# Kernel tuning notes

Hardware: AMD Instinct MI355X
Metric: run time of the kernel (lower is better)

## Reference

```python
import jax, jax.numpy as jnp
import numpy as np

B, T, C, H, K = 2, 4096, 2048, 32, 64
DM, DD, DA = 32, 64, 96
CHUNK = 128
NC = T // CHUNK
GN_EPS = 1e-5 * 8.0 ** 2  # eps * head_size_divisor**2


def setup_inputs() -> dict:
    key = jax.random.key(0)
    ks = iter(jax.random.split(key, 40))
    def nrm(shape, s=1.0):
        return jax.random.normal(next(ks), shape, dtype=jnp.float32) * s
    def uni(shape, lo, hi):
        return jax.random.uniform(next(ks), shape, dtype=jnp.float32, minval=lo, maxval=hi)
    return {
        "x": nrm((B, T, C)),
        "shift_state_in": nrm((B, C)),
        "wkv_state_in": jnp.zeros((B, H, K, K), dtype=jnp.float32),
        "time_maa_x": uni((1, 1, C), 0.0, 1.0),
        "time_maa_w": uni((1, 1, C), 0.0, 1.0),
        "time_maa_k": uni((1, 1, C), 0.0, 1.0),
        "time_maa_v": uni((1, 1, C), 0.0, 1.0),
        "time_maa_r": uni((1, 1, C), 0.0, 1.0),
        "time_maa_g": uni((1, 1, C), 0.0, 1.0),
        "time_maa_a": uni((1, 1, C), 0.0, 1.0),
        "time_maa_w1": nrm((C, 6 * DM), 0.01),
        "time_maa_w2": uni((6, DM, C), -0.01, 0.01),
        "time_decay": uni((1, 1, C), -6.0, -1.0),
        "time_decay_w1": nrm((C, DD), 0.02),
        "time_decay_w2": uni((DD, C), -0.01, 0.01),
        "time_faaaa": nrm((H, K), 0.1),
        "a0": nrm((1, 1, C), 0.01),
        "a1": nrm((C, DA), 0.02),
        "a2": nrm((DA, C), 0.1 / np.sqrt(DA)),
        "k_k": jnp.full((1, 1, C), 0.85, dtype=jnp.float32),
        "k_a": jnp.ones((1, 1, C), dtype=jnp.float32),
        "W_r": nrm((C, C), 1.0 / np.sqrt(C)),
        "W_k": nrm((C, C), 1.0 / np.sqrt(C)),
        "W_v": nrm((C, C), 1.0 / np.sqrt(C)),
        "W_g": nrm((C, C), 1.0 / np.sqrt(C)),
        "W_o": nrm((C, C), 1.0 / np.sqrt(C)),
        "gn_weight": jnp.ones((C,), dtype=jnp.float32),
        "gn_bias": jnp.zeros((C,), dtype=jnp.float32),
    }


def _wkv_delta(r, k, v, w_neg, u, kk, iclr, state0):
    # r,k,v,w_neg,kk,iclr: [B,T,C]; u: [H,K]; state0: [B,H,K,K]
    def to_chunks(t):  # [B,T,C] -> [NC,B,H,CHUNK,K]
        return t.reshape(B, NC, CHUNK, H, K).transpose(1, 0, 3, 2, 4)
    chunks = tuple(map(to_chunks, (r, k, v, w_neg, kk, iclr)))
    u4 = u.reshape(1, H, 1, K)
    mid = CHUNK // 2
    tri = jnp.tril(jnp.ones((CHUNK, CHUNK), dtype=bool), -1)
    eye = jnp.eye(CHUNK, dtype=jnp.float32)

    def step(state, chunk):
        r_c, k_c, v_c, w_log, kk_c, iclr_c = chunk
        w_cum = jnp.cumsum(w_log, axis=2)                       # [B,H,cs,K]
        w_cs = jnp.pad(w_cum[:, :, :-1, :], ((0, 0), (0, 0), (1, 0), (0, 0)))
        offset = w_cs[:, :, mid:mid + 1, :]
        r_decay = jnp.exp(jnp.clip(w_cs - offset, -30, 30))
        k_inv = jnp.exp(jnp.clip(offset - w_cum, -30, 30))
        A = jnp.einsum('bhtk,bhsk->bhts', r_c * r_decay, k_c * k_inv)
        A = jnp.where(tri, A, 0.0)
        diag = jnp.einsum('bhtk,bhtk->bht', r_c, u4 * k_c)
        A = A + diag[..., None] * eye                           # diag_embed add
        kk_corr = jnp.einsum('bhtk,bhsk->bhts', kk_c * iclr_c, kk_c)
        kk_corr = jnp.where(tri, kk_corr, 0.0)
        A_total = A - jnp.tril(A @ kk_corr)
        w_intra = jnp.exp(jnp.clip(w_cum - w_log, -30, 30))
        y = A_total @ v_c + (r_c * w_intra) @ state             # [B,H,cs,K]
        wsum = jnp.sum(w_log, axis=2, keepdims=True)            # [B,H,1,K]
        ws = jnp.exp(wsum)
        w_inter = jnp.exp(jnp.clip(wsum - w_cum, -30, 30))
        kv = jnp.einsum('bhtk,bhtv->bhkv', k_c * w_inter, v_c)
        ab = jnp.einsum('bhtk,bhtj->bhkj', -kk_c * w_inter, kk_c * iclr_c)
        state = state * ws + state @ ab + kv                    # ws broadcasts on dim -2, as in torch
        return state, y

    state, ys = jax.lax.scan(step, state0.astype(jnp.float32), chunks)
    out = ys.transpose(1, 0, 3, 2, 4).reshape(B, T, C)
    return out, state


def reference(x, shift_state_in, wkv_state_in, time_maa_x, time_maa_w, time_maa_k,
              time_maa_v, time_maa_r, time_maa_g, time_maa_a, time_maa_w1, time_maa_w2,
              time_decay, time_decay_w1, time_decay_w2, time_faaaa, a0, a1, a2,
              k_k, k_a, W_r, W_k, W_v, W_g, W_o, gn_weight, gn_bias):
    dxprev = jnp.concatenate([shift_state_in[:, None, :], x[:, :-1]], axis=1) - x
    xxx = jnp.tanh((x + dxprev * time_maa_x) @ time_maa_w1)     # [B,T,6*DM]
    m = jnp.einsum('btsd,sdc->sbtc', xxx.reshape(B, T, 6, DM), time_maa_w2)
    mw, mk, mv, mr, mg, ma = m
    xw = x + dxprev * (time_maa_w + mw)
    xk = x + dxprev * (time_maa_k + mk)
    xv = x + dxprev * (time_maa_v + mv)
    xr = x + dxprev * (time_maa_r + mr)
    xg = x + dxprev * (time_maa_g + mg)
    xa = x + dxprev * (time_maa_a + ma)
    r = xr @ W_r
    k = xk @ W_k
    v = xv @ W_v
    g = jax.nn.silu(xg @ W_g)
    w = time_decay + jnp.tanh(xw @ time_decay_w1) @ time_decay_w2
    iclr = jax.nn.sigmoid(a0 + (xa @ a1) @ a2)
    kk4 = (k * k_k).reshape(B, T, H, K)
    kk = (kk4 / jnp.maximum(jnp.linalg.norm(kk4, axis=-1, keepdims=True), 1e-12)).reshape(B, T, C)
    k = k * (1.0 + (iclr - 1.0) * k_a)
    y, wkv_state_out = _wkv_delta(r, k, v, -jnp.exp(w), time_faaaa, kk, iclr, wkv_state_in)
    # GroupNorm(H groups) over flattened tokens
    yg = y.reshape(B * T, H, K)
    mean = yg.mean(axis=-1, keepdims=True)
    var = yg.var(axis=-1, keepdims=True)
    yg = (yg - mean) / jnp.sqrt(var + GN_EPS)
    y = (yg.reshape(B * T, C) * gn_weight + gn_bias).reshape(B, T, C)
    out = (y * g) @ W_o
    return out, x[:, -1], wkv_state_out
```

## Files before the change

kernel.cpp:

```cpp
#include <hip/hip_runtime.h>


typedef unsigned short u16;
typedef unsigned int   u32;
typedef __attribute__((ext_vector_type(8))) short s16x8;
typedef __attribute__((ext_vector_type(4))) float f32x4;

#define DEV __device__ __forceinline__

DEV float b2f(u16 v){ return __uint_as_float(((u32)v) << 16); }
DEV u16 f2b(float f){ u32 u = __float_as_uint(f); return (u16)((u + 0x7fffu + ((u >> 16) & 1u)) >> 16); }
DEV float clip30(float x){ return fminf(fmaxf(x, -30.f), 30.f); }
DEV void up8(uint4 v, float* f){
  f[0]=b2f((u16)(v.x&0xffffu)); f[1]=b2f((u16)(v.x>>16));
  f[2]=b2f((u16)(v.y&0xffffu)); f[3]=b2f((u16)(v.y>>16));
  f[4]=b2f((u16)(v.z&0xffffu)); f[5]=b2f((u16)(v.z>>16));
  f[6]=b2f((u16)(v.w&0xffffu)); f[7]=b2f((u16)(v.w>>16));
}
DEV uint4 pk8(const float* f){
  uint4 v;
  v.x = (u32)f2b(f[0]) | ((u32)f2b(f[1])<<16);
  v.y = (u32)f2b(f[2]) | ((u32)f2b(f[3])<<16);
  v.z = (u32)f2b(f[4]) | ((u32)f2b(f[5])<<16);
  v.w = (u32)f2b(f[6]) | ((u32)f2b(f[7])<<16);
  return v;
}
DEV void unp16(uint4 v, u16* o){
  o[0]=(u16)(v.x&0xffffu); o[1]=(u16)(v.x>>16);
  o[2]=(u16)(v.y&0xffffu); o[3]=(u16)(v.y>>16);
  o[4]=(u16)(v.z&0xffffu); o[5]=(u16)(v.z>>16);
  o[6]=(u16)(v.w&0xffffu); o[7]=(u16)(v.w>>16);
}
DEV void gload16(const u16* g, u16* l){
  __builtin_amdgcn_global_load_lds(
      (const __attribute__((address_space(1))) u32*)g,
      (__attribute__((address_space(3))) u32*)l, 16, 0, 0);
}
#define ZF4 ((f32x4){0.f,0.f,0.f,0.f})

__global__ void transpose_k(const float* __restrict__ in, u16* __restrict__ out, int R, int C){
  __shared__ float tile[32][33];
  int c0 = blockIdx.x*32, r0 = blockIdx.y*32;
  int tx = threadIdx.x, ty = threadIdx.y;
  #pragma unroll
  for (int j=0;j<4;j++) tile[ty + j*8][tx] = in[(size_t)(r0 + ty + j*8)*C + c0 + tx];
  __syncthreads();
  #pragma unroll
  for (int j=0;j<4;j++) out[(size_t)(c0 + ty + j*8)*R + r0 + tx] = f2b(tile[tx][ty + j*8]);
}

__global__ __launch_bounds__(256) void prep_k(const float* __restrict__ x, const float* __restrict__ shift,
    const float* __restrict__ maax, u16* __restrict__ xmx, u16* __restrict__ dxp, float* __restrict__ out_xlast){
  int e8 = (blockIdx.x*256 + threadIdx.x) * 8;
  int row = e8 >> 11, col = e8 & 2047;
  int t = row & 4095, b = row >> 12;
  const float* xp = x + (size_t)row*2048 + col;
  const float* pp = t ? (x + (size_t)(row-1)*2048 + col) : (shift + (size_t)b*2048 + col);
  float xf[8], pf[8], mf[8], of[8], df[8];
  *(float4*)(xf)   = *(const float4*)(xp);
  *(float4*)(xf+4) = *(const float4*)(xp+4);
  *(float4*)(pf)   = *(const float4*)(pp);
  *(float4*)(pf+4) = *(const float4*)(pp+4);
  *(float4*)(mf)   = *(const float4*)(maax + col);
  *(float4*)(mf+4) = *(const float4*)(maax + col + 4);
  #pragma unroll
  for (int j=0;j<8;j++){ df[j] = pf[j]-xf[j]; of[j] = xf[j] + df[j]*mf[j]; }
  *(uint4*)(xmx + (size_t)row*2048 + col) = pk8(of);
  *(uint4*)(dxp + (size_t)row*2048 + col) = pk8(df);
  if (t == 4095){
    *(float4*)(out_xlast + (size_t)b*2048 + col)     = *(const float4*)(xf);
    *(float4*)(out_xlast + (size_t)b*2048 + col + 4) = *(const float4*)(xf+4);
  }
}

enum { EPI_STORE=0, EPI_TANH=1, EPI_SILU=2, EPI_LERP=3, EPI_ICLR=5, EPI_STORE32=6 };

__global__ __launch_bounds__(256) void lerp6_k(
    const u16* __restrict__ xxx, const u16* __restrict__ w2t,
    const float* __restrict__ x, const u16* __restrict__ dxp,
    const float* __restrict__ ma0, const float* __restrict__ ma1, const float* __restrict__ ma2,
    const float* __restrict__ ma3, const float* __restrict__ ma4, const float* __restrict__ ma5,
    u16* __restrict__ o0, u16* __restrict__ o1, u16* __restrict__ o2,
    u16* __restrict__ o3, u16* __restrict__ o4, u16* __restrict__ o5)
{
  __shared__ u16 As[128][40];
  __shared__ u16 Bs[128][40];
  const int tid = threadIdx.x, lane = tid & 63, wid = tid >> 6;
  const int m0 = blockIdx.x*128, n0 = blockIdx.y*128;
  const int wrow = (wid>>1)*64, wcol = (wid&1)*64;
  const int fr = lane&15, kg = lane>>4;
  const int r_c0 = tid>>2, r_seg = tid&3, r_c1 = r_c0+64;
  const float* maap[6] = {ma0,ma1,ma2,ma3,ma4,ma5};
  u16* outs[6] = {o0,o1,o2,o3,o4,o5};

  float xv_[4][4][4], dxv_[4][4][4];
  #pragma unroll
  for (int m=0;m<4;m++)
    #pragma unroll
    for (int n=0;n<4;n++)
      #pragma unroll
      for (int q=0;q<4;q++){
        int row = m0 + wrow + m*16 + kg*4 + q;
        int col = n0 + wcol + n*16 + fr;
        xv_[m][n][q]  = x[(size_t)row*2048 + col];
        dxv_[m][n][q] = b2f(dxp[(size_t)row*2048 + col]);
      }

  #pragma unroll
  for (int s=0;s<6;s++){
    __syncthreads();
    *(uint4*)(&As[r_c0][r_seg*8]) = *(const uint4*)(xxx + (size_t)(m0+r_c0)*192 + s*32 + r_seg*8);
    *(uint4*)(&As[r_c1][r_seg*8]) = *(const uint4*)(xxx + (size_t)(m0+r_c1)*192 + s*32 + r_seg*8);
    *(uint4*)(&Bs[r_c0][r_seg*8]) = *(const uint4*)(w2t + (size_t)(n0+r_c0)*192 + s*32 + r_seg*8);
    *(uint4*)(&Bs[r_c1][r_seg*8]) = *(const uint4*)(w2t + (size_t)(n0+r_c1)*192 + s*32 + r_seg*8);
    __syncthreads();
    s16x8 a[4], bb[4];
    #pragma unroll
    for (int m=0;m<4;m++) a[m] = *(const s16x8*)(&As[wrow + m*16 + fr][kg*8]);
    #pragma unroll
    for (int n=0;n<4;n++) bb[n] = *(const s16x8*)(&Bs[wcol + n*16 + fr][kg*8]);
    f32x4 acc[4][4];
    #pragma unroll
    for (int m=0;m<4;m++)
      #pragma unroll
      for (int n=0;n<4;n++) acc[m][n] = ZF4;
    #pragma unroll
    for (int m=0;m<4;m++)
      #pragma unroll
      for (int n=0;n<4;n++)
        acc[m][n] = __builtin_amdgcn_mfma_f32_16x16x32_bf16(a[m], bb[n], acc[m][n], 0,0,0);
    #pragma unroll
    for (int n=0;n<4;n++){
      int col = n0 + wcol + n*16 + fr;
      float mv = maap[s][col];
      #pragma unroll
      for (int m=0;m<4;m++)
        #pragma unroll
        for (int q=0;q<4;q++){
          int row = m0 + wrow + m*16 + kg*4 + q;
          outs[s][(size_t)row*2048 + col] = f2b(xv_[m][n][q] + dxv_[m][n][q]*(mv + acc[m][n][q]));
        }
    }
  }
}

template<int EPI>
__global__ __launch_bounds__(512, 2) void gemm256_k(
    const u16* __restrict__ A, const u16* __restrict__ Bt,
    u16* __restrict__ Cout, float* __restrict__ Cout32,
    int M, int N, int K)
{
  __shared__ __align__(16) u16 lds[4*16384];
  const int tid = threadIdx.x, lane = tid & 63;
  int bxx = blockIdx.x, byy = blockIdx.y;
  if (gridDim.x == 32 && gridDim.y == 8){
    int bid = byy * 32 + bxx;
    int xcd = bid & 7, idx = bid >> 3;
    bxx = xcd*4 + (idx & 3);
    byy = idx >> 2;
  } else {
    int nwg = gridDim.x * gridDim.y;
    if ((nwg & 7) == 0){
      int bid = byy * gridDim.x + bxx;
      int cpx = nwg >> 3;
      int swz = (bid & 7) * cpx + (bid >> 3);
      bxx = swz % gridDim.x; byy = swz / gridDim.x;
    }
  }
  const int m0 = bxx * 256, n0 = byy * 256;
  const int wid = tid >> 6;
  const int wm = wid >> 2, wn = wid & 3;
  const int fr = lane & 15, kg = lane >> 4;
  const int NT = K >> 5;
  const int chunk0 = __builtin_amdgcn_readfirstlane(wid) * 2;
  const int lr = lane >> 2, lsl = lane & 3;
  const int gswz = (lsl ^ ((lr >> 1) & 3)) << 3;
  const int kswz = (kg ^ ((fr >> 1) & 3)) << 3;

  f32x4 acc[8][4];
  #pragma unroll
  for (int m=0;m<8;m++)
    #pragma unroll
    for (int n=0;n<4;n++) acc[m][n] = ZF4;

  auto STAGE = [&](int t){
    u16* ab = lds + (t & 3) * 16384;
    u16* bb = ab + 8192;
    int gc = (t << 5) + gswz;
    #pragma unroll
    for (int i=0;i<2;i++){
      int c = chunk0 + i;
      int r = c*16 + lr;
      gload16(A  + (size_t)(m0 + r)*K + gc, ab + c*512);
      gload16(Bt + (size_t)(n0 + r)*K + gc, bb + c*512);
    }
  };

  STAGE(0); STAGE(1); STAGE(2);
  for (int t=0; t<NT; ++t){
    asm volatile("s_waitcnt vmcnt(8)" ::: "memory");
    __builtin_amdgcn_s_barrier();
    __builtin_amdgcn_sched_barrier(0);
    if (t+3 < NT) STAGE(t+3);
    const u16* ab = lds + (t & 3) * 16384;
    const u16* bb = ab + 8192;
    s16x8 af[8], bf[4];
    #pragma unroll
    for (int m=0;m<8;m++){
      int r = wm*128 + m*16 + fr;
      af[m] = *(const s16x8*)(ab + r*32 + kswz);
    }
    #pragma unroll
    for (int n=0;n<4;n++){
      int r = wn*64 + n*16 + fr;
      bf[n] = *(const s16x8*)(bb + r*32 + kswz);
    }
    __builtin_amdgcn_s_setprio(1);
    #pragma unroll
    for (int m=0;m<8;m++)
      #pragma unroll
      for (int n=0;n<4;n++)
        acc[m][n] = __builtin_amdgcn_mfma_f32_16x16x32_bf16(af[m], bf[n], acc[m][n], 0,0,0);
    __builtin_amdgcn_s_setprio(0);
  }

  #pragma unroll
  for (int n=0;n<4;n++){
    int ccol = n0 + wn*64 + n*16 + fr;
    #pragma unroll
    for (int m=0;m<8;m++){
      #pragma unroll
      for (int q=0;q<4;q++){
        int row = m0 + wm*128 + m*16 + kg*4 + q;
        float v = acc[m][n][q];
        size_t oidx = (size_t)row*N + ccol;
        if constexpr (EPI == EPI_STORE) Cout[oidx] = f2b(v);
        else if constexpr (EPI == EPI_STORE32) Cout32[oidx] = v;
        else if constexpr (EPI == EPI_SILU) Cout[oidx] = f2b(v / (1.f + __expf(-v)));
      }
    }
  }
}

template<int EPI, bool ASYNC, bool SWZ>
__global__ __launch_bounds__(256) void gemm_k(
    const u16* __restrict__ A, int lda,
    const u16* __restrict__ Bt, int ldb,
    u16* __restrict__ Cout, float* __restrict__ Cout32, int ldc,
    int M, int N, int K,
    const float* __restrict__ e_x, const u16* __restrict__ e_dxp, const float* __restrict__ e_vec)
{
  constexpr int LDW = ASYNC ? 32 : 40;
  __shared__ u16 As[128][LDW];
  __shared__ u16 Bs[128][LDW];
  const int tid = threadIdx.x;
  const int lane = tid & 63, wid = tid >> 6;
  int bxx = blockIdx.x, byy = blockIdx.y;
  if constexpr (SWZ){
    int nwg = gridDim.x * gridDim.y;
    if ((nwg & 7) == 0){
      int bid = byy * gridDim.x + bxx;
      int cpx = nwg >> 3;
      int swz = (bid & 7) * cpx + (bid >> 3);
      bxx = swz % gridDim.x; byy = swz / gridDim.x;
    }
  }
  const int m0 = bxx * 128, n0 = byy * 128;
  const int wrow = (wid >> 1) * 64, wcol = (wid & 1) * 64;
  const int fr = lane & 15, kg = lane >> 4;
  const int r_c0 = tid >> 2, r_seg = tid & 3;
  const int r_c1 = r_c0 + 64;

  f32x4 acc[4][4];
  #pragma unroll
  for (int m=0;m<4;m++)
    #pragma unroll
    for (int n=0;n<4;n++) acc[m][n] = ZF4;

  for (int k0 = 0; k0 < K; k0 += 32) {
    __syncthreads();
    if constexpr (ASYNC) {
      const int w4 = __builtin_amdgcn_readfirstlane(wid);
      const int rr = lane >> 2, seg8 = (lane & 3) * 8;
      #pragma unroll
      for (int i=0;i<2;i++){
        int row = w4*32 + i*16 + rr;
        gload16(A  + (size_t)(m0 + row)*lda + k0 + seg8, &As[w4*32 + i*16][0]);
        gload16(Bt + (size_t)(n0 + row)*ldb + k0 + seg8, &Bs[w4*32 + i*16][0]);
      }
    } else {
      uint4 av0 = *(const uint4*)(A + (size_t)(m0 + r_c0)*lda + k0 + r_seg*8);
      uint4 av1 = *(const uint4*)(A + (size_t)(m0 + r_c1)*lda + k0 + r_seg*8);
      *(uint4*)(&As[r_c0][r_seg*8]) = av0;
      *(uint4*)(&As[r_c1][r_seg*8]) = av1;
      uint4 z = make_uint4(0,0,0,0);
      uint4 bv0 = (n0 + r_c0 < N) ? *(const uint4*)(Bt + (size_t)(n0 + r_c0)*ldb + k0 + r_seg*8) : z;
      uint4 bv1 = (n0 + r_c1 < N) ? *(const uint4*)(Bt + (size_t)(n0 + r_c1)*ldb + k0 + r_seg*8) : z;
      *(uint4*)(&Bs[r_c0][r_seg*8]) = bv0;
      *(uint4*)(&Bs[r_c1][r_seg*8]) = bv1;
    }
    __syncthreads();
    s16x8 a[4], bb[4];
    #pragma unroll
    for (int m=0;m<4;m++) a[m] = *(const s16x8*)(&As[wrow + m*16 + fr][kg*8]);
    #pragma unroll
    for (int n=0;n<4;n++) bb[n] = *(const s16x8*)(&Bs[wcol + n*16 + fr][kg*8]);
    #pragma unroll
    for (int m=0;m<4;m++)
      #pragma unroll
      for (int n=0;n<4;n++)
        acc[m][n] = __builtin_amdgcn_mfma_f32_16x16x32_bf16(a[m], bb[n], acc[m][n], 0,0,0);
  }
  #pragma unroll
  for (int n=0;n<4;n++){
    int ccol = n0 + wcol + n*16 + fr;
    if (ccol >= N) continue;
    #pragma unroll
    for (int m=0;m<4;m++){
      #pragma unroll
      for (int q=0;q<4;q++){
        int row = m0 + wrow + m*16 + kg*4 + q;
        float v = acc[m][n][q];
        size_t oidx = (size_t)row*ldc + ccol;
        if constexpr (EPI == EPI_STORE) Cout[oidx] = f2b(v);
        else if constexpr (EPI == EPI_STORE32) Cout32[oidx] = v;
        else if constexpr (EPI == EPI_TANH) Cout[oidx] = f2b(tanhf(v));
        else if constexpr (EPI == EPI_SILU) Cout[oidx] = f2b(v / (1.f + expf(-v)));
        else if constexpr (EPI == EPI_LERP){
          float xv = e_x[(size_t)row*2048 + ccol];
          float dx = b2f(e_dxp[(size_t)row*2048 + ccol]);
          Cout[oidx] = f2b(xv + dx * (e_vec[ccol] + v));
        }
        else if constexpr (EPI == EPI_ICLR) Cout[oidx] = f2b(1.f / (1.f + expf(-(e_vec[ccol] + v))));
      }
    }
  }
}

template<int EPI>
__global__ __launch_bounds__(256) void gemm_thin_k(
    const u16* __restrict__ A, int lda,
    const u16* __restrict__ Bt, int ldb,
    u16* __restrict__ Cout, int ldc, int N, int K)
{
  __shared__ u16 As[64][72];
  __shared__ u16 Bs[64][72];
  const int tid = threadIdx.x;
  const int lane = tid & 63, wid = tid >> 6;
  const int m0 = blockIdx.x * 64, n0 = blockIdx.y * 64;
  const int wrow = (wid >> 1) * 32, wcol = (wid & 1) * 32;
  const int fr = lane & 15, kg = lane >> 4;
  const int r_c = tid >> 2, r_seg = tid & 3;

  f32x4 acc[2][2];
  #pragma unroll
  for (int m=0;m<2;m++)
    #pragma unroll
    for (int n=0;n<2;n++) acc[m][n] = ZF4;

  for (int k0 = 0; k0 < K; k0 += 64) {
    __syncthreads();
    {
      const u16* as = A + (size_t)(m0 + r_c)*lda + k0 + r_seg*16;
      *(uint4*)(&As[r_c][r_seg*16])     = *(const uint4*)(as);
      *(uint4*)(&As[r_c][r_seg*16 + 8]) = *(const uint4*)(as + 8);
      uint4 z = make_uint4(0,0,0,0);
      bool ok = (n0 + r_c < N);
      const u16* bs = Bt + (size_t)(n0 + r_c)*ldb + k0 + r_seg*16;
      *(uint4*)(&Bs[r_c][r_seg*16])     = ok ? *(const uint4*)(bs) : z;
      *(uint4*)(&Bs[r_c][r_seg*16 + 8]) = ok ? *(const uint4*)(bs + 8) : z;
    }
    __syncthreads();
    #pragma unroll
    for (int ks=0; ks<2; ++ks){
      s16x8 a[2], bb[2];
      #pragma unroll
      for (int m=0;m<2;m++) a[m] = *(const s16x8*)(&As[wrow + m*16 + fr][ks*32 + kg*8]);
      #pragma unroll
      for (int n=0;n<2;n++) bb[n] = *(const s16x8*)(&Bs[wcol + n*16 + fr][ks*32 + kg*8]);
      #pragma unroll
      for (int m=0;m<2;m++)
        #pragma unroll
        for (int n=0;n<2;n++)
          acc[m][n] = __builtin_amdgcn_mfma_f32_16x16x32_bf16(a[m], bb[n], acc[m][n], 0,0,0);
    }
  }
  #pragma unroll
  for (int n=0;n<2;n++){
    int ccol = n0 + wcol + n*16 + fr;
    if (ccol >= N) continue;
    #pragma unroll
    for (int m=0;m<2;m++){
      #pragma unroll
      for (int q=0;q<4;q++){
        int row = m0 + wrow + m*16 + kg*4 + q;
        float v = acc[m][n][q];
        size_t oidx = (size_t)row*ldc + ccol;
        if constexpr (EPI == EPI_TANH) Cout[oidx] = f2b(tanhf(v));
        else Cout[oidx] = f2b(v);
      }
    }
  }
}

__global__ __launch_bounds__(512, 1) void wkv1_k(
    const u16* __restrict__ r_g, const u16* __restrict__ kraw_g, const u16* __restrict__ v_g,
    const u16* __restrict__ ic_g,
    const u16* __restrict__ t2_g, const u16* __restrict__ dw2t_g, const float* __restrict__ td_g,
    const float* __restrict__ u_g, const float* __restrict__ kkk_g, const float* __restrict__ kka_g,
    u16* __restrict__ y1_g, u16* __restrict__ rw_g,
    u16* __restrict__ kvab_g, float* __restrict__ wsA_g)
{
  __shared__ __align__(16) char arena[162304];
  float* WL   = (float*)(arena);
  float* WC   = (float*)(arena + 34816);
  u16* Abuf   = (u16*)(arena);
  u16* kkcT   = (u16*)(arena + 34816);
  float* diag_l = (float*)(arena + 68096);
  float* offs_l = diag_l + 128;
  float* wsum_l = offs_l + 64;
  float* u_l    = wsum_l + 64;
  float* kkk_l  = u_l + 64;
  float* kka_l  = kkk_l + 64;
  float* td_l   = kka_l + 64;
  u16* rd_l   = (u16*)(arena + 70144);
  u16* vT_l   = (u16*)(arena + 70144);
  u16* ki_l   = (u16*)(arena + 88576);
  u16* kkwT_l = (u16*)(arena + 88576);
  u16* kwT_l  = (u16*)(arena + 107008);
  u16* ka_l   = (u16*)(arena + 125440);
  u16* kkb_l  = (u16*)(arena + 143872);
  u16* kaT_l  = (u16*)(arena + 143872);

  const int tid = threadIdx.x, lane = tid & 63, wid = tid >> 6;
  const int cb = blockIdx.x;
  const int c = cb >> 6, b = (cb >> 5) & 1, h = cb & 31;
  const size_t base = ((size_t)(b*4096 + c*128)) * 2048 + h*64;
  const int fr = lane & 15, kg = lane >> 4;
  const int tq = tid >> 2, kh = (tid & 3) * 16;

  const u16* g_rs = r_g    + base + (size_t)tq*2048 + kh;
  const u16* g_ks = kraw_g + base + (size_t)tq*2048 + kh;
  const u16* g_is = ic_g   + base + (size_t)tq*2048 + kh;
  const u16* g_vs = v_g    + base + (size_t)tq*2048 + kh;
  uint4 pfr0 = *(const uint4*)(g_rs), pfr1 = *(const uint4*)(g_rs + 8);
  uint4 pfk0 = *(const uint4*)(g_ks), pfk1 = *(const uint4*)(g_ks + 8);
  uint4 pfi0 = *(const uint4*)(g_is), pfi1 = *(const uint4*)(g_is + 8);
  uint4 pfv0 = *(const uint4*)(g_vs), pfv1 = *(const uint4*)(g_vs + 8);

  {
    const u16* t2s = t2_g + (size_t)(b*4096 + c*128 + tq)*64 + kh;
    *(uint4*)(&rd_l[tq*72 + kh])     = *(const uint4*)(t2s);
    *(uint4*)(&rd_l[tq*72 + kh + 8]) = *(const uint4*)(t2s + 8);
    int n = tid >> 3, sg2 = (tid & 7) * 8;
    *(uint4*)(&ki_l[n*72 + sg2]) = *(const uint4*)(dw2t_g + (size_t)(h*64 + n)*64 + sg2);
  }
  if (tid < 64){
    u_l[tid]   = u_g[h*64 + tid];
    kkk_l[tid] = kkk_g[h*64 + tid];
    kka_l[tid] = kka_g[h*64 + tid];
    td_l[tid]  = td_g[h*64 + tid];
  }
  __syncthreads();
  {
    f32x4 accW[4];
    #pragma unroll
    for (int n=0;n<4;n++) accW[n] = ZF4;
    #pragma unroll
    for (int ks=0; ks<2; ++ks){
      s16x8 af = *(const s16x8*)(&rd_l[(wid*16 + fr)*72 + ks*32 + kg*8]);
      #pragma unroll
      for (int n=0;n<4;n++){
        s16x8 bf = *(const s16x8*)(&ki_l[(n*16 + fr)*72 + ks*32 + kg*8]);
        accW[n] = __builtin_amdgcn_mfma_f32_16x16x32_bf16(af, bf, accW[n], 0,0,0);
      }
    }
    #pragma unroll
    for (int n=0;n<4;n++)
      #pragma unroll
      for (int q=0;q<4;q++){
        int t = wid*16 + kg*4 + q;
        int s = n*16 + fr;
        WL[t*65 + s] = -__expf(td_l[s] + accW[n][q]);
      }
  }
  __syncthreads();
  for (int j=0;j<8;j++){
    int k = wid*8 + j;
    float v = WL[lane*65 + k];
    #pragma unroll
    for (int d=1; d<64; d<<=1){ float o = __shfl_up(v, d); if (lane >= d) v += o; }
    WC[lane*65 + k] = v;
    float carry = __shfl(v, 63);
    float v2 = WL[(64+lane)*65 + k];
    #pragma unroll
    for (int d=1; d<64; d<<=1){ float o = __shfl_up(v2, d); if (lane >= d) v2 += o; }
    v2 += carry;
    WC[(64+lane)*65 + k] = v2;
    float tot = __shfl(v2, 63);
    if (lane == 0){ offs_l[k] = carry; wsum_l[k] = tot; wsA_g[(size_t)cb*64 + k] = __expf(tot); }
  }
  __syncthreads();
  {
    float dpart = 0.f;
    #pragma unroll
    for (int j=0;j<2;j++){
      float rf[8], kf[8], icf[8], rdf[8], kif[8], rwf[8];
      up8(j ? pfr1 : pfr0, rf);
      up8(j ? pfk1 : pfk0, kf);
      up8(j ? pfi1 : pfi0, icf);
      #pragma unroll
      for (int e=0;e<8;e++){
        int k = kh + j*8 + e;
        float kadj = kf[e] * (1.f + (icf[e] - 1.f) * kka_l[k]);
        float wl = WL[tq*65+k], wc = WC[tq*65+k];
        float wcs = wc - wl;
        float off = offs_l[k], wsm = wsum_l[k];
        rdf[e] = rf[e] * __expf(clip30(wcs - off));
        kif[e] = kadj  * __expf(clip30(off - wc));
        rwf[e] = rf[e] * __expf(clip30(wcs));
        kwT_l[k*136 + tq] = f2b(kadj * __expf(clip30(wsm - wc)));
        dpart += rf[e] * u_l[k] * kadj;
      }
      *(uint4*)(&rd_l[tq*72 + kh + j*8]) = pk8(rdf);
      *(uint4*)(&ki_l[tq*72 + kh + j*8]) = pk8(kif);
      *(uint4*)(rw_g + base + (size_t)tq*2048 + kh + j*8) = pk8(rwf);
    }
    dpart += __shfl_xor(dpart, 1);
    dpart += __shfl_xor(dpart, 2);
    if ((tid & 3) == 0) diag_l[tq] = dpart;
  }
  __syncthreads();
  {
    float kf[16], icf[16], kkraw[16];
    up8(pfk0, kf); up8(pfk1, kf + 8);
    up8(pfi0, icf); up8(pfi1, icf + 8);
    float ss = 0.f;
    #pragma unroll
    for (int e=0;e<16;e++){ kkraw[e] = kf[e]*kkk_l[kh+e]; ss += kkraw[e]*kkraw[e]; }
    ss += __shfl_xor(ss, 1);
    ss += __shfl_xor(ss, 2);
    float rn = 1.f / fmaxf(sqrtf(ss), 1e-12f);
    #pragma unroll
    for (int j=0;j<2;j++){
      float kkb8[8], ka8[8];
      #pragma unroll
      for (int e=0;e<8;e++){
        float kkv = kkraw[j*8+e]*rn;
        kkb8[e] = kkv; ka8[e] = kkv*icf[j*8+e];
      }
      *(uint4*)(&kkb_l[tq*72 + kh + j*8]) = pk8(kkb8);
      *(uint4*)(&ka_l [tq*72 + kh + j*8]) = pk8(ka8);
    }
  }
  __syncthreads();
  f32x4 accA[8];
  #pragma unroll
  for (int n=0;n<8;n++) accA[n] = ZF4;
  #pragma unroll
  for (int ks=0; ks<2; ++ks){
    s16x8 af = *(const s16x8*)(&rd_l[(wid*16 + fr)*72 + ks*32 + kg*8]);
    #pragma unroll
    for (int n=0;n<8;n++){
      s16x8 bf = *(const s16x8*)(&ki_l[(n*16 + fr)*72 + ks*32 + kg*8]);
      accA[n] = __builtin_amdgcn_mfma_f32_16x16x32_bf16(af, bf, accA[n], 0,0,0);
    }
  }
  #pragma unroll
  for (int n=0;n<8;n++)
    #pragma unroll
    for (int q=0;q<4;q++){
      int t = wid*16 + kg*4 + q;
      int s = n*16 + fr;
      float v = accA[n][q];
      v = (t > s) ? v : ((t == s) ? diag_l[t] : 0.f);
      accA[n][q] = v;
      Abuf[t*136 + s] = f2b(v);
    }
  __syncthreads();
  {
    #pragma unroll
    for (int j=0;j<2;j++){
      float kkf[8];
      up8(*(const uint4*)(&kkb_l[tq*72 + kh + j*8]), kkf);
      #pragma unroll
      for (int e=0;e<8;e++){
        int k = kh + j*8 + e;
        kkwT_l[k*136 + tq] = f2b(-kkf[e] * __expf(clip30(wsum_l[k] - WC[tq*65+k])));
      }
    }
  }
  __syncthreads();
  {
    f32x4 accC[8];
    #pragma unroll
    for (int n=0;n<8;n++) accC[n] = ZF4;
    #pragma unroll
    for (int ks=0; ks<2; ++ks){
      s16x8 af = *(const s16x8*)(&ka_l[(wid*16 + fr)*72 + ks*32 + kg*8]);
      #pragma unroll
      for (int n=0;n<8;n++){
        s16x8 bf = *(const s16x8*)(&kkb_l[(n*16 + fr)*72 + ks*32 + kg*8]);
        accC[n] = __builtin_amdgcn_mfma_f32_16x16x32_bf16(af, bf, accC[n], 0,0,0);
      }
    }
    #pragma unroll
    for (int n=0;n<8;n++)
      #pragma unroll
      for (int q=0;q<4;q++){
        int t = wid*16 + kg*4 + q;
        int s = n*16 + fr;
        kkcT[s*136 + t] = f2b((t > s) ? accC[n][q] : 0.f);
      }
  }
  __syncthreads();
  {
    u16 el[8];
    unp16(pfv0, el);
    #pragma unroll
    for (int e=0;e<8;e++) vT_l[(kh + e)*136 + tq] = el[e];
    unp16(pfv1, el);
    #pragma unroll
    for (int e=0;e<8;e++) vT_l[(kh + 8 + e)*136 + tq] = el[e];
    #pragma unroll
    for (int j=0;j<2;j++){
      u16 el2[8]; unp16(*(const uint4*)(&ka_l[tq*72 + kh + j*8]), el2);
      #pragma unroll
      for (int e=0;e<8;e++) kaT_l[(kh + j*8 + e)*136 + tq] = el2[e];
    }
  }
  {
    f32x4 accP[8];
    #pragma unroll
    for (int n=0;n<8;n++) accP[n] = ZF4;
    #pragma unroll
    for (int ks=0; ks<4; ++ks){
      s16x8 af = *(const s16x8*)(&Abuf[(wid*16 + fr)*136 + ks*32 + kg*8]);
      #pragma unroll
      for (int n=0;n<8;n++){
        s16x8 bf = *(const s16x8*)(&kkcT[(n*16 + fr)*136 + ks*32 + kg*8]);
        accP[n] = __builtin_amdgcn_mfma_f32_16x16x32_bf16(af, bf, accP[n], 0,0,0);
      }
    }
    #pragma unroll
    for (int n=0;n<8;n++)
      #pragma unroll
      for (int q=0;q<4;q++){
        int t = wid*16 + kg*4 + q;
        int s = n*16 + fr;
        float v = accA[n][q] - ((t >= s) ? accP[n][q] : 0.f);
        Abuf[t*136 + s] = f2b(v);
      }
  }
  __syncthreads();
  {
    f32x4 accY[4];
    #pragma unroll
    for (int n=0;n<4;n++) accY[n] = ZF4;
    #pragma unroll
    for (int ks=0; ks<4; ++ks){
      s16x8 af = *(const s16x8*)(&Abuf[(wid*16 + fr)*136 + ks*32 + kg*8]);
      #pragma unroll
      for (int n=0;n<4;n++){
        s16x8 bf = *(const s16x8*)(&vT_l[(n*16 + fr)*136 + ks*32 + kg*8]);
        accY[n] = __builtin_amdgcn_mfma_f32_16x16x32_bf16(af, bf, accY[n], 0,0,0);
      }
    }
    #pragma unroll
    for (int n=0;n<4;n++)
      #pragma unroll
      for (int q=0;q<4;q++){
        int t = wid*16 + kg*4 + q;
        int vd = n*16 + fr;
        y1_g[base + (size_t)t*2048 + vd] = f2b(accY[n][q]);
      }
  }
  {
    const int isAB = wid >> 2, mrow = (wid & 3) * 16;
    const u16* Amat = isAB ? kkwT_l : kwT_l;
    const u16* Bmat = isAB ? kaT_l  : vT_l;
    f32x4 acc2[4];
    #pragma unroll
    for (int n=0;n<4;n++) acc2[n] = ZF4;
    #pragma unroll
    for (int ks=0; ks<4; ++ks){
      s16x8 af = *(const s16x8*)(&Amat[(mrow + fr)*136 + ks*32 + kg*8]);
      #pragma unroll
      for (int n=0;n<4;n++){
        s16x8 bf = *(const s16x8*)(&Bmat[(n*16 + fr)*136 + ks*32 + kg*8]);
        acc2[n] = __builtin_amdgcn_mfma_f32_16x16x32_bf16(af, bf, acc2[n], 0,0,0);
      }
    }
    u16* kvp = kvab_g + (size_t)cb*8192 + isAB*4096;
    #pragma unroll
    for (int n=0;n<4;n++)
      #pragma unroll
      for (int q=0;q<4;q++){
        int kd = mrow + kg*4 + q, vd = n*16 + fr;
        if (isAB) kvp[vd*64 + kd] = f2b(acc2[n][q]);
        else      kvp[kd*64 + vd] = f2b(acc2[n][q]);
      }
  }
}

__global__ __launch_bounds__(256) void wkv2_k(
   const float* __restrict__ state_in, u16* __restrict__ kvab_g,
   const float* __restrict__ wsA_g, float* __restrict__ out_state)
{
  __shared__ u16 Sb[64][72];
  __shared__ u16 abT[64][72];
  const int tid = threadIdx.x, lane = tid & 63, wid = tid >> 6;
  const int bh = blockIdx.x, b = bh >> 5, h = bh & 31;
  const int fr = lane & 15, kg = lane >> 4;
  const int r0 = wid*16 + kg*4;
  const int vrow = tid >> 2, jc = (tid & 3) * 16;

  f32x4 S[4];
  #pragma unroll
  for (int n=0;n<4;n++)
    #pragma unroll
    for (int q=0;q<4;q++)
      S[n][q] = state_in[(size_t)bh*4096 + (size_t)(r0+q)*64 + n*16+fr];

  uint4 pf_ab0, pf_ab1; u16 pf_kv[16]; float pf_ws[4];
  {
    int cb = b*32 + h;
    const u16* kvp = kvab_g + (size_t)cb*8192;
    pf_ab0 = *(const uint4*)(kvp + 4096 + vrow*64 + jc);
    pf_ab1 = *(const uint4*)(kvp + 4096 + vrow*64 + jc + 8);
    #pragma unroll
    for (int n=0;n<4;n++)
      #pragma unroll
      for (int q=0;q<4;q++)
        pf_kv[n*4+q] = kvp[(r0+q)*64 + n*16+fr];
    #pragma unroll
    for (int n=0;n<4;n++) pf_ws[n] = wsA_g[(size_t)cb*64 + n*16+fr];
  }

  for (int c=0;c<32;c++){
    int cb = (c*2+b)*32 + h;
    *(uint4*)(&abT[vrow][jc])   = pf_ab0;
    *(uint4*)(&abT[vrow][jc+8]) = pf_ab1;
    #pragma unroll
    for (int n=0;n<4;n++)
      #pragma unroll
      for (int q=0;q<4;q++)
        Sb[r0+q][n*16+fr] = f2b(S[n][q]);
    float kvf[16], wsf[4];
    #pragma unroll
    for (int i=0;i<16;i++) kvf[i] = b2f(pf_kv[i]);
    #pragma unroll
    for (int n=0;n<4;n++) wsf[n] = pf_ws[n];
    float* sip = (float*)(kvab_g + (size_t)cb*8192);
    #pragma unroll
    for (int n=0;n<4;n++)
      #pragma unroll
      for (int q=0;q<4;q++)
        sip[(r0+q)*64 + n*16+fr] = S[n][q];
    __syncthreads();
    if (c < 31){
      int cb2 = ((c+1)*2+b)*32 + h;
      const u16* kvp2 = kvab_g + (size_t)cb2*8192;
      pf_ab0 = *(const uint4*)(kvp2 + 4096 + vrow*64 + jc);
      pf_ab1 = *(const uint4*)(kvp2 + 4096 + vrow*64 + jc + 8);
      #pragma unroll
      for (int n=0;n<4;n++)
        #pragma unroll
        for (int q=0;q<4;q++)
          pf_kv[n*4+q] = kvp2[(r0+q)*64 + n*16+fr];
      #pragma unroll
      for (int n=0;n<4;n++) pf_ws[n] = wsA_g[(size_t)cb2*64 + n*16+fr];
    }
    f32x4 acc[4];
    #pragma unroll
    for (int n=0;n<4;n++) acc[n] = ZF4;
    #pragma unroll
    for (int ks=0; ks<2; ++ks){
      s16x8 a = *(const s16x8*)(&Sb[wid*16 + fr][ks*32 + kg*8]);
      #pragma unroll
      for (int n=0;n<4;n++){
        s16x8 bb = *(const s16x8*)(&abT[n*16 + fr][ks*32 + kg*8]);
        acc[n] = __builtin_amdgcn_mfma_f32_16x16x32_bf16(a, bb, acc[n], 0,0,0);
      }
    }
    #pragma unroll
    for (int n=0;n<4;n++)
      #pragma unroll
      for (int q=0;q<4;q++)
        S[n][q] = S[n][q]*wsf[n] + acc[n][q] + kvf[n*4+q];
    __syncthreads();
  }
  #pragma unroll
  for (int n=0;n<4;n++)
    #pragma unroll
    for (int q=0;q<4;q++)
      out_state[(size_t)bh*4096 + (size_t)(r0+q)*64 + n*16+fr] = S[n][q];
}

__global__ __launch_bounds__(256) void wkv3_k(
   const u16* __restrict__ y1_g, const u16* __restrict__ rw_g,
   const u16* __restrict__ kvab_g,
   const u16* __restrict__ g_g, const float* __restrict__ gnw, const float* __restrict__ gnb,
   u16* __restrict__ yf_g)
{
  __shared__ float S_l[64][65];
  __shared__ u16 rw_l[128][72];
  int tid = threadIdx.x;
  int cb = blockIdx.x; int c = cb>>6, b = (cb>>5)&1, h = cb&31;
  size_t base = ((size_t)(b*4096 + c*128))*2048 + h*64;
  const float* sip = (const float*)(kvab_g + (size_t)cb*8192);
  #pragma unroll
  for (int j=0;j<16;j++){ int flat = tid*16+j; S_l[flat>>6][flat&63] = sip[flat]; }
  {
    int t = tid>>1, kh = (tid&1)*32;
    const u16* rs = rw_g + base + (size_t)t*2048 + kh;
    #pragma unroll
    for (int j=0;j<4;j++) *(uint4*)(&rw_l[t][kh+j*8]) = *(const uint4*)(rs + j*8);
  }
  __syncthreads();
  int t = tid>>1, vh = (tid&1)*32;
  float acc[32];
  #pragma unroll
  for (int j=0;j<32;j++) acc[j] = 0.f;
  for (int kf2=0; kf2<64; kf2++){
    float rv = b2f(rw_l[t][kf2]);
    #pragma unroll
    for (int j=0;j<32;j++) acc[j] += rv * S_l[kf2][vh+j];
  }
  float sum=0.f, sq=0.f;
  float yv[32];
  #pragma unroll
  for (int j=0;j<32;j++){
    yv[j] = acc[j] + b2f(y1_g[base + (size_t)t*2048 + vh + j]);
    sum += yv[j]; sq += yv[j]*yv[j];
  }
  sum += __shfl_xor(sum, 1); sq += __shfl_xor(sq, 1);
  float mean = sum * (1.f/64.f);
  float var = sq * (1.f/64.f) - mean*mean;
  float rstd = rsqrtf(fmaxf(var, 0.f) + 6.4e-4f);
  size_t bt = (size_t)(b*4096 + c*128 + t);
  #pragma unroll
  for (int j=0;j<32;j++){
    int ch = h*64 + vh + j;
    float val = (yv[j]-mean)*rstd * gnw[ch] + gnb[ch];
    val *= b2f(g_g[bt*2048 + ch]);
    yf_g[base + (size_t)t*2048 + vh + j] = f2b(val);
  }
}

#define O_WTR   0ull
#define O_WTK   8388608ull
#define O_WTV   16777216ull
#define O_WTG   25165824ull
#define O_WTO   33554432ull
#define O_W1T   41943040ull
#define O_W2T   42729472ull
#define O_DW1T  43515904ull
#define O_DW2T  43778048ull
#define O_A1T   44040192ull
#define O_A2T   44433408ull
#define O_XXX   44826624ull
#define O_T2    47972352ull
#define O_T3    49020928ull
#define O_WSA   50593792ull
#define O_XMX   51118080ull
#define O_A     84672512ull
#define O_I     118226944ull
#define O_R     151781376ull
#define O_K     185335808ull
#define O_V     218890240ull
#define WS_NEEDED 252444672ull

extern "C" void kernel_launch(void* const* d_in, const int* in_sizes, int n_in,
                              void* d_out, int out_size, void* d_ws, size_t ws_size,
                              hipStream_t stream)
{
  (void)in_sizes; (void)n_in; (void)out_size;
  if (ws_size < WS_NEEDED) return;
  const float* x     = (const float*)d_in[0];
  const float* shift = (const float*)d_in[1];
  const float* st_in = (const float*)d_in[2];
  const float* maax  = (const float*)d_in[3];
  const float* maas[6] = {(const float*)d_in[4],(const float*)d_in[5],(const float*)d_in[6],
                          (const float*)d_in[7],(const float*)d_in[8],(const float*)d_in[9]};
  const float* w1    = (const float*)d_in[10];
  const float* w2    = (const float*)d_in[11];
  const float* td    = (const float*)d_in[12];
  const float* dw1   = (const float*)d_in[13];
  const float* dw2   = (const float*)d_in[14];
  const float* faaaa = (const float*)d_in[15];
  const float* a0v   = (const float*)d_in[16];
  const float* a1w   = (const float*)d_in[17];
  const float* a2w   = (const float*)d_in[18];
  const float* kkk   = (const float*)d_in[19];
  const float* kka   = (const float*)d_in[20];
  const float* Wr    = (const float*)d_in[21];
  const float* Wk    = (const float*)d_in[22];
  const float* Wv    = (const float*)d_in[23];
  const float* Wg    = (const float*)d_in[24];
  const float* Wo    = (const float*)d_in[25];
  const float* gnw   = (const float*)d_in[26];
  const float* gnb   = (const float*)d_in[27];
  float* out = (float*)d_out;
  char* ws = (char*)d_ws;
  #define WSP(o) ((u16*)(ws + (o)))

  u16 *wtR=WSP(O_WTR), *wtK=WSP(O_WTK), *wtV=WSP(O_WTV), *wtG=WSP(O_WTG), *wtO=WSP(O_WTO);
  u16 *w1t=WSP(O_W1T), *w2t=WSP(O_W2T), *dw1t=WSP(O_DW1T), *dw2t=WSP(O_DW2T), *a1t=WSP(O_A1T), *a2t=WSP(O_A2T);
  u16 *xxx=WSP(O_XXX), *t2b=WSP(O_T2), *t3b=WSP(O_T3);
  u16 *sXMX=WSP(O_XMX), *sA=WSP(O_A), *sI=WSP(O_I), *sR=WSP(O_R), *sK=WSP(O_K), *sV=WSP(O_V);
  u16 *rw = WSP(O_WTR);
  float* wsA = (float*)(ws + O_WSA);
  float* out_xlast = out + 16777216;
  float* out_state = out + 16781312;

  dim3 tb(32,8);
  transpose_k<<<dim3(64,64), tb, 0, stream>>>(Wr, wtR, 2048, 2048);
  transpose_k<<<dim3(64,64), tb, 0, stream>>>(Wk, wtK, 2048, 2048);
  transpose_k<<<dim3(64,64), tb, 0, stream>>>(Wv, wtV, 2048, 2048);
  transpose_k<<<dim3(64,64), tb, 0, stream>>>(Wg, wtG, 2048, 2048);
  transpose_k<<<dim3(64,64), tb, 0, stream>>>(Wo, wtO, 2048, 2048);
  transpose_k<<<dim3(6,64),  tb, 0, stream>>>(w1, w1t, 2048, 192);
  transpose_k<<<dim3(64,6),  tb, 0, stream>>>(w2, w2t, 192, 2048);
  transpose_k<<<dim3(2,64),  tb, 0, stream>>>(dw1, dw1t, 2048, 64);
  transpose_k<<<dim3(64,2),  tb, 0, stream>>>(dw2, dw2t, 64, 2048);
  transpose_k<<<dim3(3,64),  tb, 0, stream>>>(a1w, a1t, 2048, 96);
  transpose_k<<<dim3(64,3),  tb, 0, stream>>>(a2w, a2t, 96, 2048);

  prep_k<<<8192, 256, 0, stream>>>(x, shift, maax, sXMX , sI , out_xlast);

  gemm_thin_k<EPI_TANH><<<dim3(128,3), 256, 0, stream>>>(sXMX, 2048, w1t, 2048, xxx, 192, 192, 2048);
  lerp6_k<<<dim3(64,16), 256, 0, stream>>>(xxx, w2t, x, sI ,
      maas[0], maas[1], maas[2], maas[3], maas[4], maas[5],
      sXMX , sA , sR , sK , sV , sI );
  gemm_thin_k<EPI_TANH><<<dim3(128,1), 256, 0, stream>>>(sXMX, 2048, dw1t, 2048, t2b, 64, 64, 2048);
  gemm_thin_k<EPI_STORE><<<dim3(128,2), 256, 0, stream>>>(sI, 2048, a1t, 2048, t3b, 96, 96, 2048);
  gemm_k<EPI_ICLR,true,true><<<dim3(64,16), 256, 0, stream>>>(t3b, 96, a2t, 96, sI, nullptr, 2048, 8192, 2048, 96, nullptr, nullptr, a0v);
  gemm256_k<EPI_STORE><<<dim3(32,8), 512, 0, stream>>>(sK, wtR, sXMX, nullptr, 8192, 2048, 2048);
  gemm256_k<EPI_STORE><<<dim3(32,8), 512, 0, stream>>>(sA, wtK, sK, nullptr, 8192, 2048, 2048);
  gemm256_k<EPI_STORE><<<dim3(32,8), 512, 0, stream>>>(sR, wtV, sA, nullptr, 8192, 2048, 2048);
  gemm256_k<EPI_SILU><<<dim3(32,8), 512, 0, stream>>>(sV, wtG, sR, nullptr, 8192, 2048, 2048);
  wkv1_k<<<2048, 512, 0, stream>>>(sXMX, sK, sA, sI, t2b, dw2t, td, faaaa, kkk, kka,
                                   sK, rw, sV, wsA);
  wkv2_k<<<64, 256, 0, stream>>>(st_in, sV, wsA, out_state);
  wkv3_k<<<2048, 256, 0, stream>>>(sK, rw, sV, sR , gnw, gnb, sK );
  gemm256_k<EPI_STORE32><<<dim3(32,8), 512, 0, stream>>>(sK, wtO, nullptr, out, 8192, 2048, 2048);
}
```

Baseline: 995.0 us.

## Split wkv2 state scan across row groups, batch weight transposes, defer wkv1 loads

The sequential inter-chunk state scan (wkv2) previously ran on only 64 blocks, one per batch-head. It now runs on 256 blocks, each owning 16 rows of the 64x64 state, so every wave does a single MFMA per step instead of four. Per-chunk input states now go to a separate fp32 buffer that reuses the dead XMX workspace, because the in-place kvab storage would race across the row-group blocks. The five large weight transposes are merged into one 3D-grid launch, and the up-front r/k/ic/v prefetch registers in wkv1 are replaced with loads at point of use, which lowers register pressure but removes the latency hiding.

```diff
diff --git a/kernel.cpp b/kernel.cpp
--- a/kernel.cpp
+++ b/kernel.cpp
@@ -47,6 +47,24 @@
   __syncthreads();
   #pragma unroll
   for (int j=0;j<4;j++) out[(size_t)(c0 + ty + j*8)*R + r0 + tx] = f2b(tile[tx][ty + j*8]);
+}
+
+__global__ void transpose5_k(const float* __restrict__ w0, const float* __restrict__ w1,
+    const float* __restrict__ w2, const float* __restrict__ w3, const float* __restrict__ w4,
+    u16* __restrict__ o0, u16* __restrict__ o1, u16* __restrict__ o2,
+    u16* __restrict__ o3, u16* __restrict__ o4){
+  __shared__ float tile[32][33];
+  const float* ins[5] = {w0,w1,w2,w3,w4};
+  u16* outs[5] = {o0,o1,o2,o3,o4};
+  const float* in = ins[blockIdx.z];
+  u16* out = outs[blockIdx.z];
+  int c0 = blockIdx.x*32, r0 = blockIdx.y*32;
+  int tx = threadIdx.x, ty = threadIdx.y;
+  #pragma unroll
+  for (int j=0;j<4;j++) tile[ty + j*8][tx] = in[(size_t)(r0 + ty + j*8)*2048 + c0 + tx];
+  __syncthreads();
+  #pragma unroll
+  for (int j=0;j<4;j++) out[(size_t)(c0 + ty + j*8)*2048 + r0 + tx] = f2b(tile[tx][ty + j*8]);
 }
 
 __global__ __launch_bounds__(256) void prep_k(const float* __restrict__ x, const float* __restrict__ shift,
@@ -439,15 +457,6 @@
   const int fr = lane & 15, kg = lane >> 4;
   const int tq = tid >> 2, kh = (tid & 3) * 16;
 
-  const u16* g_rs = r_g    + base + (size_t)tq*2048 + kh;
-  const u16* g_ks = kraw_g + base + (size_t)tq*2048 + kh;
-  const u16* g_is = ic_g   + base + (size_t)tq*2048 + kh;
-  const u16* g_vs = v_g    + base + (size_t)tq*2048 + kh;
-  uint4 pfr0 = *(const uint4*)(g_rs), pfr1 = *(const uint4*)(g_rs + 8);
-  uint4 pfk0 = *(const uint4*)(g_ks), pfk1 = *(const uint4*)(g_ks + 8);
-  uint4 pfi0 = *(const uint4*)(g_is), pfi1 = *(const uint4*)(g_is + 8);
-  uint4 pfv0 = *(const uint4*)(g_vs), pfv1 = *(const uint4*)(g_vs + 8);
-
   {
     const u16* t2s = t2_g + (size_t)(b*4096 + c*128 + tq)*64 + kh;
     *(uint4*)(&rd_l[tq*72 + kh])     = *(const uint4*)(t2s);
@@ -502,13 +511,16 @@
   }
   __syncthreads();
   {
+    const u16* rs  = r_g    + base + (size_t)tq*2048 + kh;
+    const u16* ks_ = kraw_g + base + (size_t)tq*2048 + kh;
+    const u16* is_ = ic_g   + base + (size_t)tq*2048 + kh;
     float dpart = 0.f;
     #pragma unroll
     for (int j=0;j<2;j++){
       float rf[8], kf[8], icf[8], rdf[8], kif[8], rwf[8];
-      up8(j ? pfr1 : pfr0, rf);
-      up8(j ? pfk1 : pfk0, kf);
-      up8(j ? pfi1 : pfi0, icf);
+      up8(*(const uint4*)(rs + j*8), rf);
+      up8(*(const uint4*)(ks_ + j*8), kf);
+      up8(*(const uint4*)(is_ + j*8), icf);
       #pragma unroll
       for (int e=0;e<8;e++){
         int k = kh + j*8 + e;
@@ -532,9 +544,14 @@
   }
   __syncthreads();
   {
+    const u16* ks_ = kraw_g + base + (size_t)tq*2048 + kh;
+    const u16* is_ = ic_g   + base + (size_t)tq*2048 + kh;
     float kf[16], icf[16], kkraw[16];
-    up8(pfk0, kf); up8(pfk1, kf + 8);
-    up8(pfi0, icf); up8(pfi1, icf + 8);
+    #pragma unroll
+    for (int j=0;j<2;j++){
+      up8(*(const uint4*)(ks_ + j*8), kf + j*8);
+      up8(*(const uint4*)(is_ + j*8), icf + j*8);
+    }
     float ss = 0.f;
     #pragma unroll
     for (int e=0;e<16;e++){ kkraw[e] = kf[e]*kkk_l[kh+e]; ss += kkraw[e]*kkraw[e]; }
@@ -615,13 +632,13 @@
   }
   __syncthreads();
   {
-    u16 el[8];
-    unp16(pfv0, el);
-    #pragma unroll
-    for (int e=0;e<8;e++) vT_l[(kh + e)*136 + tq] = el[e];
-    unp16(pfv1, el);
-    #pragma unroll
-    for (int e=0;e<8;e++) vT_l[(kh + 8 + e)*136 + tq] = el[e];
+    const u16* vs = v_g + base + (size_t)tq*2048 + kh;
+    #pragma unroll
+    for (int j=0;j<2;j++){
+      u16 el[8]; unp16(*(const uint4*)(vs + j*8), el);
+      #pragma unroll
+      for (int e=0;e<8;e++) vT_l[(kh + j*8 + e)*136 + tq] = el[e];
+    }
     #pragma unroll
     for (int j=0;j<2;j++){
       u16 el2[8]; unp16(*(const uint4*)(&ka_l[tq*72 + kh + j*8]), el2);
@@ -704,37 +721,35 @@
 }
 
 __global__ __launch_bounds__(256) void wkv2_k(
-   const float* __restrict__ state_in, u16* __restrict__ kvab_g,
-   const float* __restrict__ wsA_g, float* __restrict__ out_state)
+   const float* __restrict__ state_in, const u16* __restrict__ kvab_g,
+   const float* __restrict__ wsA_g, float* __restrict__ sin_g, float* __restrict__ out_state)
 {
-  __shared__ u16 Sb[64][72];
+  __shared__ u16 Sb[16][72];
   __shared__ u16 abT[64][72];
   const int tid = threadIdx.x, lane = tid & 63, wid = tid >> 6;
-  const int bh = blockIdx.x, b = bh >> 5, h = bh & 31;
+  const int blk = blockIdx.x;
+  const int bh = blk >> 2, rg = blk & 3;
+  const int b = bh >> 5, h = bh & 31;
   const int fr = lane & 15, kg = lane >> 4;
-  const int r0 = wid*16 + kg*4;
+  const int lrow = kg*4;
+  const int grow = rg*16 + lrow;
+  const int vcol = wid*16 + fr;
   const int vrow = tid >> 2, jc = (tid & 3) * 16;
 
-  f32x4 S[4];
-  #pragma unroll
-  for (int n=0;n<4;n++)
-    #pragma unroll
-    for (int q=0;q<4;q++)
-      S[n][q] = state_in[(size_t)bh*4096 + (size_t)(r0+q)*64 + n*16+fr];
-
-  uint4 pf_ab0, pf_ab1; u16 pf_kv[16]; float pf_ws[4];
+  f32x4 S;
+  #pragma unroll
+  for (int q=0;q<4;q++)
+    S[q] = state_in[(size_t)bh*4096 + (size_t)(grow+q)*64 + vcol];
+
+  uint4 pf_ab0, pf_ab1; u16 pf_kv[4]; float pf_ws;
   {
     int cb = b*32 + h;
     const u16* kvp = kvab_g + (size_t)cb*8192;
     pf_ab0 = *(const uint4*)(kvp + 4096 + vrow*64 + jc);
     pf_ab1 = *(const uint4*)(kvp + 4096 + vrow*64 + jc + 8);
     #pragma unroll
-    for (int n=0;n<4;n++)
-      #pragma unroll
-      for (int q=0;q<4;q++)
-        pf_kv[n*4+q] = kvp[(r0+q)*64 + n*16+fr];
-    #pragma unroll
-    for (int n=0;n<4;n++) pf_ws[n] = wsA_g[(size_t)cb*64 + n*16+fr];
+    for (int q=0;q<4;q++) pf_kv[q] = kvp[(grow+q)*64 + vcol];
+    pf_ws = wsA_g[(size_t)cb*64 + vcol];
   }
 
   for (int c=0;c<32;c++){
@@ -742,21 +757,14 @@
     *(uint4*)(&abT[vrow][jc])   = pf_ab0;
     *(uint4*)(&abT[vrow][jc+8]) = pf_ab1;
     #pragma unroll
-    for (int n=0;n<4;n++)
-      #pragma unroll
-      for (int q=0;q<4;q++)
-        Sb[r0+q][n*16+fr] = f2b(S[n][q]);
-    float kvf[16], wsf[4];
-    #pragma unroll
-    for (int i=0;i<16;i++) kvf[i] = b2f(pf_kv[i]);
-    #pragma unroll
-    for (int n=0;n<4;n++) wsf[n] = pf_ws[n];
-    float* sip = (float*)(kvab_g + (size_t)cb*8192);
-    #pragma unroll
-    for (int n=0;n<4;n++)
-      #pragma unroll
-      for (int q=0;q<4;q++)
-        sip[(r0+q)*64 + n*16+fr] = S[n][q];
+    for (int q=0;q<4;q++) Sb[lrow+q][vcol] = f2b(S[q]);
+    float kvf[4];
+    #pragma unroll
+    for (int q=0;q<4;q++) kvf[q] = b2f(pf_kv[q]);
+    float wsf = pf_ws;
+    float* sip = sin_g + (size_t)cb*4096;
+    #pragma unroll
+    for (int q=0;q<4;q++) sip[(size_t)(grow+q)*64 + vcol] = S[q];
     __syncthreads();
     if (c < 31){
       int cb2 = ((c+1)*2+b)*32 + h;
@@ -764,42 +772,29 @@
       pf_ab0 = *(const uint4*)(kvp2 + 4096 + vrow*64 + jc);
       pf_ab1 = *(const uint4*)(kvp2 + 4096 + vrow*64 + jc + 8);
       #pragma unroll
-      for (int n=0;n<4;n++)
-        #pragma unroll
-        for (int q=0;q<4;q++)
-          pf_kv[n*4+q] = kvp2[(r0+q)*64 + n*16+fr];
-      #pragma unroll
-      for (int n=0;n<4;n++) pf_ws[n] = wsA_g[(size_t)cb2*64 + n*16+fr];
-    }
-    f32x4 acc[4];
-    #pragma unroll
-    for (int n=0;n<4;n++) acc[n] = ZF4;
+      for (int q=0;q<4;q++) pf_kv[q] = kvp2[(grow+q)*64 + vcol];
+      pf_ws = wsA_g[(size_t)cb2*64 + vcol];
+    }
+    f32x4 acc = ZF4;
     #pragma unroll
     for (int ks=0; ks<2; ++ks){
-      s16x8 a = *(const s16x8*)(&Sb[wid*16 + fr][ks*32 + kg*8]);
-      #pragma unroll
-      for (int n=0;n<4;n++){
-        s16x8 bb = *(const s16x8*)(&abT[n*16 + fr][ks*32 + kg*8]);
-        acc[n] = __builtin_amdgcn_mfma_f32_16x16x32_bf16(a, bb, acc[n], 0,0,0);
-      }
-    }
-    #pragma unroll
-    for (int n=0;n<4;n++)
-      #pragma unroll
-      for (int q=0;q<4;q++)
-        S[n][q] = S[n][q]*wsf[n] + acc[n][q] + kvf[n*4+q];
+      s16x8 a  = *(const s16x8*)(&Sb[fr][ks*32 + kg*8]);
+      s16x8 bb = *(const s16x8*)(&abT[wid*16 + fr][ks*32 + kg*8]);
+      acc = __builtin_amdgcn_mfma_f32_16x16x32_bf16(a, bb, acc, 0,0,0);
+    }
+    #pragma unroll
+    for (int q=0;q<4;q++)
+      S[q] = S[q]*wsf + acc[q] + kvf[q];
     __syncthreads();
   }
   #pragma unroll
-  for (int n=0;n<4;n++)
-    #pragma unroll
-    for (int q=0;q<4;q++)
-      out_state[(size_t)bh*4096 + (size_t)(r0+q)*64 + n*16+fr] = S[n][q];
+  for (int q=0;q<4;q++)
+    out_state[(size_t)bh*4096 + (size_t)(grow+q)*64 + vcol] = S[q];
 }
 
 __global__ __launch_bounds__(256) void wkv3_k(
    const u16* __restrict__ y1_g, const u16* __restrict__ rw_g,
-   const u16* __restrict__ kvab_g,
+   const float* __restrict__ sin_g,
    const u16* __restrict__ g_g, const float* __restrict__ gnw, const float* __restrict__ gnb,
    u16* __restrict__ yf_g)
 {
@@ -808,7 +803,7 @@
   int tid = threadIdx.x;
   int cb = blockIdx.x; int c = cb>>6, b = (cb>>5)&1, h = cb&31;
   size_t base = ((size_t)(b*4096 + c*128))*2048 + h*64;
-  const float* sip = (const float*)(kvab_g + (size_t)cb*8192);
+  const float* sip = sin_g + (size_t)cb*4096;
   #pragma unroll
   for (int j=0;j<16;j++){ int flat = tid*16+j; S_l[flat>>6][flat&63] = sip[flat]; }
   {
@@ -910,16 +905,13 @@
   u16 *xxx=WSP(O_XXX), *t2b=WSP(O_T2), *t3b=WSP(O_T3);
   u16 *sXMX=WSP(O_XMX), *sA=WSP(O_A), *sI=WSP(O_I), *sR=WSP(O_R), *sK=WSP(O_K), *sV=WSP(O_V);
   u16 *rw = WSP(O_WTR);
+  float* sinF = (float*)(ws + O_XMX);
   float* wsA = (float*)(ws + O_WSA);
   float* out_xlast = out + 16777216;
   float* out_state = out + 16781312;
 
   dim3 tb(32,8);
-  transpose_k<<<dim3(64,64), tb, 0, stream>>>(Wr, wtR, 2048, 2048);
-  transpose_k<<<dim3(64,64), tb, 0, stream>>>(Wk, wtK, 2048, 2048);
-  transpose_k<<<dim3(64,64), tb, 0, stream>>>(Wv, wtV, 2048, 2048);
-  transpose_k<<<dim3(64,64), tb, 0, stream>>>(Wg, wtG, 2048, 2048);
-  transpose_k<<<dim3(64,64), tb, 0, stream>>>(Wo, wtO, 2048, 2048);
+  transpose5_k<<<dim3(64,64,5), tb, 0, stream>>>(Wr, Wk, Wv, Wg, Wo, wtR, wtK, wtV, wtG, wtO);
   transpose_k<<<dim3(6,64),  tb, 0, stream>>>(w1, w1t, 2048, 192);
   transpose_k<<<dim3(64,6),  tb, 0, stream>>>(w2, w2t, 192, 2048);
   transpose_k<<<dim3(2,64),  tb, 0, stream>>>(dw1, dw1t, 2048, 64);
@@ -942,7 +934,7 @@
   gemm256_k<EPI_SILU><<<dim3(32,8), 512, 0, stream>>>(sV, wtG, sR, nullptr, 8192, 2048, 2048);
   wkv1_k<<<2048, 512, 0, stream>>>(sXMX, sK, sA, sI, t2b, dw2t, td, faaaa, kkk, kka,
                                    sK, rw, sV, wsA);
-  wkv2_k<<<64, 256, 0, stream>>>(st_in, sV, wsA, out_state);
-  wkv3_k<<<2048, 256, 0, stream>>>(sK, rw, sV, sR , gnw, gnb, sK );
+  wkv2_k<<<256, 256, 0, stream>>>(st_in, sV, wsA, sinF, out_state);
+  wkv3_k<<<2048, 256, 0, stream>>>(sK, rw, sinF, sR , gnw, gnb, sK );
   gemm256_k<EPI_STORE32><<<dim3(32,8), 512, 0, stream>>>(sK, wtO, nullptr, out, 8192, 2048, 2048);
 }
```

After: 970.1 us. 2.5% less time.
